# Optimization experiments

Hardware: AMD Instinct MI355X
Metric: run time of the kernel (lower is better)

## Reference

```python
import jax, jax.numpy as jnp
import numpy as np

NX, NY, D, K = 20000, 50000, 64, 8
NUM_BATCHES = 2


def _knn_np(px, py, bx, by, k):
    # Batched exact kNN via chunked squared-distance + argpartition (mirrors torch_cluster.knn under no_grad).
    pp = (px * px).sum(1)
    idx = np.empty((py.shape[0], k), np.int32)
    chunk = 4096
    for s in range(0, py.shape[0], chunk):
        q = py[s:s + chunk]
        d = (q * q).sum(1)[:, None] + pp[None, :] - 2.0 * (q @ px.T)
        d = np.where(by[s:s + chunk, None] == bx[None, :], d, np.inf)
        idx[s:s + chunk] = np.argpartition(d, k, axis=1)[:, :k].astype(np.int32)
    return idx


def setup_inputs() -> dict:
    rng = np.random.default_rng(0)
    pos_x = (rng.random((NX, 3)) * 10.0).astype(np.float32)
    pos_y = (rng.random((NY, 3)) * 10.0).astype(np.float32)
    bx = np.repeat(np.arange(NUM_BATCHES), NX // NUM_BATCHES).astype(np.int32)
    by = np.repeat(np.arange(NUM_BATCHES), NY // NUM_BATCHES).astype(np.int32)
    x_idx = _knn_np(pos_x, pos_y, bx, by, K).reshape(-1)            # [NY*K]
    y_idx = np.repeat(np.arange(NY, dtype=np.int32), K)             # [NY*K]

    key = jax.random.key(0)
    ks = jax.random.split(key, 6)

    def lin(k, fi, fo):
        return jax.random.normal(k, (fi, fo), jnp.float32) / np.sqrt(fi).astype(np.float32)

    return {
        "x": jax.random.normal(ks[0], (NX, D), jnp.float32),
        "pos_x": jnp.asarray(pos_x),
        "pos_y": jnp.asarray(pos_y),
        "x_idx": jnp.asarray(x_idx),
        "y_idx": jnp.asarray(y_idx),
        # ResnetBlockFC 1: size_in=D+3, size_h=D, size_out=D (shortcut linear, no bias)
        "W0a": lin(ks[1], D + 3, D), "b0a": jnp.zeros((D,), jnp.float32),
        "W1a": lin(ks[2], D, D),     "b1a": jnp.zeros((D,), jnp.float32),
        "Wsa": lin(ks[3], D + 3, D),
        # ResnetBlockFC 2: size_in=size_h=size_out=D (identity shortcut)
        "W0b": lin(ks[4], D, D),     "b0b": jnp.zeros((D,), jnp.float32),
        "W1b": lin(ks[5], D, D),     "b1b": jnp.zeros((D,), jnp.float32),
    }


def reference(x, pos_x, pos_y, x_idx, y_idx, W0a, b0a, W1a, b1a, Wsa, W0b, b0b, W1b, b1b):
    # gather + positional diff (diff computed under no_grad in the original)
    diff = jax.lax.stop_gradient(pos_x[x_idx] - pos_y[y_idx])        # [E, 3]
    h = jnp.concatenate([x[x_idx], diff], axis=1)                    # [E, D+3]
    # ResnetBlockFC 1: out = shortcut(h) + fc1(relu(fc0(relu(h))))
    net = jax.nn.relu(h) @ W0a + b0a
    dx = jax.nn.relu(net) @ W1a + b1a
    h = h @ Wsa + dx                                                 # [E, D]
    # ResnetBlockFC 2 (identity shortcut)
    net = jax.nn.relu(h) @ W0b + b0b
    h = h + jax.nn.relu(net) @ W1b + b1b                             # [E, D]
    # scatter-max back to query points (every query has exactly K edges)
    out = jax.ops.segment_max(h, y_idx, num_segments=NY)             # [NY, D]
    return out
```

## Files before the change

kernel.cpp:

```cpp
#include <hip/hip_runtime.h>


typedef _Float16 f16x8 __attribute__((ext_vector_type(8)));
typedef _Float16 f16x4 __attribute__((ext_vector_type(4)));
typedef float    f32x4 __attribute__((ext_vector_type(4)));

constexpr int NX     = 20000;
constexpr int NROWS  = 50000 * 8;
constexpr int NTILES = NROWS / 16;
constexpr int NFRAG  = 48;
constexpr int BW     = 8;
constexpr int BLOCK  = 64 * BW;
constexpr int TS2    = 72;

__global__ void prep_x(const float* __restrict__ x, _Float16* __restrict__ x16) {
    const int i = blockIdx.x * blockDim.x + threadIdx.x;
    if (i < NX * 16) {
        float4 v = ((const float4*)x)[i];
        f16x4 o = {(_Float16)v.x, (_Float16)v.y, (_Float16)v.z, (_Float16)v.w};
        *(f16x4*)(x16 + (size_t)i * 4) = o;
    }
}

static __device__ __forceinline__ void pack_relu(const f32x4* A, f16x8* bf) {
#pragma unroll
    for (int s = 0; s < 2; ++s) {
        f16x8 r;
#pragma unroll
        for (int e = 0; e < 8; ++e) {
            float v = A[2 * s + (e >> 2)][e & 3];
            r[e] = (_Float16)(v > 0.0f ? v : 0.0f);
        }
        bf[s] = r;
    }
}

__global__ __launch_bounds__(BLOCK, 4)
void pointnet_fused(const _Float16* __restrict__ x16,
                    const float* __restrict__ pos_x,
                    const float* __restrict__ pos_y,
                    const int*   __restrict__ x_idx,
                    const float* __restrict__ W0a, const float* __restrict__ b0a,
                    const float* __restrict__ W1a, const float* __restrict__ b1a,
                    const float* __restrict__ Wsa,
                    const float* __restrict__ W0b, const float* __restrict__ b0b,
                    const float* __restrict__ W1b, const float* __restrict__ b1b,
                    float* __restrict__ out)
{
    __shared__ __align__(16) _Float16 bfrag[NFRAG * 64 * 8];
    __shared__ __align__(16) _Float16 ebuf[BW][16 * TS2];
    __shared__ __align__(16) float    bias3f[64];
    __shared__ __align__(16) float    bias5f[64];

    const int tid = threadIdx.x;

    for (int p = tid; p < NFRAG * 64; p += BLOCK) {
        const int f = p >> 6, l = p & 63;
        const int q = l >> 4, n0 = l & 15;
        int grp, fl;
        if      (f < 12) { grp = 0; fl = f; }
        else if (f < 24) { grp = 1; fl = f - 12; }
        else if (f < 32) { grp = 2; fl = f - 24; }
        else if (f < 40) { grp = 3; fl = f - 32; }
        else             { grp = 4; fl = f - 40; }
        const int s = fl >> 2, t = fl & 3;
        const int col = t * 16 + n0;
        f16x8 v;
#pragma unroll
        for (int j = 0; j < 8; ++j) {
            const int k = 32 * s + 8 * q + j;
            float val = 0.0f;
            if      (grp == 0) val = (k < 67) ? W0a[k * 64 + col] : (k == 67 ? b0a[col] : 0.0f);
            else if (grp == 1) val = (k < 67) ? Wsa[k * 64 + col] : (k == 67 ? b1a[col] : 0.0f);
            else {
                const float* W = (grp == 2) ? W1a : (grp == 3) ? W0b : W1b;
                const int row = 32 * s + 16 * (j >> 2) + 4 * q + (j & 3);
                val = W[row * 64 + col];
            }
            v[j] = (_Float16)val;
        }
        *(f16x8*)&bfrag[p * 8] = v;
    }
    if (tid < 64)       bias3f[tid]      = b0b[tid];
    else if (tid < 128) bias5f[tid - 64] = b1b[tid - 64];
    __syncthreads();

    const int lane = tid & 63;
    const int wv   = tid >> 6;
    const int n0   = lane & 15;
    const int q    = lane >> 4;

    _Float16* eb = ebuf[wv];

    const int ey  = (lane >> 3) & 1;
    const int efg = lane & 7;
    const int esb = lane >> 4;

    const int gwave  = blockIdx.x * BW + wv;
    const int nwaves = gridDim.x * BW;

#define WFRAG(fid) (*(const f16x8*)&bfrag[(((fid) * 64) + lane) * 8])

    f16x8 hc0, hc1, hc2;
    {
        const int row = gwave * 16 + n0;
        const int xi  = x_idx[row];
        const _Float16* xp = x16 + (long)xi * 64 + q * 8;
        hc0 = *(const f16x8*)(xp);
        hc1 = *(const f16x8*)(xp + 32);
        f16x8 z = {}; hc2 = z;
        if (q == 0) {
            const int yi = row >> 3;
#pragma unroll
            for (int j = 0; j < 3; ++j)
                hc2[j] = (_Float16)(pos_x[xi * 3 + j] - pos_y[yi * 3 + j]);
            hc2[3] = (_Float16)1.0f;
        }
    }

    for (int tile = gwave; tile < NTILES; tile += nwaves) {
        const int tnx  = tile + nwaves;
        const int rown = (tnx < NTILES ? tnx : tile) * 16 + n0;
        const int xin  = x_idx[rown];
        const int yin  = rown >> 3;
        const float py0 = pos_y[yin * 3 + 0];
        const float py1 = pos_y[yin * 3 + 1];
        const float py2 = pos_y[yin * 3 + 2];

        f16x8 hr0 = hc0, hr1 = hc1, hr2 = hc2;
#pragma unroll
        for (int j = 0; j < 8; ++j) {
            hr0[j] = hr0[j] > (_Float16)0 ? hr0[j] : (_Float16)0;
            hr1[j] = hr1[j] > (_Float16)0 ? hr1[j] : (_Float16)0;
            hr2[j] = hr2[j] > (_Float16)0 ? hr2[j] : (_Float16)0;
        }

        f32x4 A1[4], A2[4];
#pragma unroll
        for (int t = 0; t < 4; ++t) {
            A1[t] = (f32x4){0.f, 0.f, 0.f, 0.f};
            A2[t] = (f32x4){0.f, 0.f, 0.f, 0.f};
        }
        {
            const f16x8 hcs[3] = {hc0, hc1, hc2};
            const f16x8 hrs[3] = {hr0, hr1, hr2};
#pragma unroll
            for (int s = 0; s < 3; ++s)
#pragma unroll
                for (int t = 0; t < 4; ++t) {
                    A2[t] = __builtin_amdgcn_mfma_f32_16x16x32_f16(WFRAG(12 + s * 4 + t), hcs[s], A2[t], 0, 0, 0);
                    A1[t] = __builtin_amdgcn_mfma_f32_16x16x32_f16(WFRAG( 0 + s * 4 + t), hrs[s], A1[t], 0, 0, 0);
                }
        }

        f16x8 hn0, hn1, hn2;
        {
            const _Float16* xp = x16 + (long)xin * 64 + q * 8;
            hn0 = *(const f16x8*)(xp);
            hn1 = *(const f16x8*)(xp + 32);
            f16x8 z = {}; hn2 = z;
            if (q == 0) {
                hn2[0] = (_Float16)(pos_x[xin * 3 + 0] - py0);
                hn2[1] = (_Float16)(pos_x[xin * 3 + 1] - py1);
                hn2[2] = (_Float16)(pos_x[xin * 3 + 2] - py2);
                hn2[3] = (_Float16)1.0f;
            }
        }

        f16x8 bf[2];
        pack_relu(A1, bf);
#pragma unroll
        for (int s = 0; s < 2; ++s)
#pragma unroll
            for (int t = 0; t < 4; ++t)
                A2[t] = __builtin_amdgcn_mfma_f32_16x16x32_f16(WFRAG(24 + s * 4 + t), bf[s], A2[t], 0, 0, 0);

        pack_relu(A2, bf);
        f32x4 A3[4];
#pragma unroll
        for (int t = 0; t < 4; ++t) A3[t] = *(const f32x4*)&bias3f[16 * t + 4 * q];
#pragma unroll
        for (int s = 0; s < 2; ++s)
#pragma unroll
            for (int t = 0; t < 4; ++t)
                A3[t] = __builtin_amdgcn_mfma_f32_16x16x32_f16(WFRAG(32 + s * 4 + t), bf[s], A3[t], 0, 0, 0);

        pack_relu(A3, bf);
#pragma unroll
        for (int s = 0; s < 2; ++s)
#pragma unroll
            for (int t = 0; t < 4; ++t)
                A2[t] = __builtin_amdgcn_mfma_f32_16x16x32_f16(WFRAG(40 + s * 4 + t), bf[s], A2[t], 0, 0, 0);

        __threadfence_block();
#pragma unroll
        for (int t = 0; t < 4; ++t) {
            f16x4 w;
#pragma unroll
            for (int r = 0; r < 4; ++r) w[r] = (_Float16)A2[t][r];
            *(f16x4*)&eb[n0 * TS2 + t * 16 + q * 4] = w;
        }
        __threadfence_block();

        const int dr0 = ey * 8 + esb * 2;
        f16x8 ra = *(const f16x8*)&eb[dr0 * TS2 + efg * 8];
        f16x8 rb = *(const f16x8*)&eb[(dr0 + 1) * TS2 + efg * 8];
#pragma unroll
        for (int e = 0; e < 8; ++e) ra[e] = ra[e] > rb[e] ? ra[e] : rb[e];
#pragma unroll
        for (int st = 0; st < 2; ++st) {
            union { f16x8 h; int i[4]; } u, v2;
            u.h = ra;
#pragma unroll
            for (int d = 0; d < 4; ++d) v2.i[d] = __shfl_xor(u.i[d], st == 0 ? 16 : 32, 64);
#pragma unroll
            for (int e = 0; e < 8; ++e) ra[e] = ra[e] > v2.h[e] ? ra[e] : v2.h[e];
        }
        if (esb == 0) {
            const f32x4 bb0 = *(const f32x4*)&bias5f[efg * 8];
            const f32x4 bb1 = *(const f32x4*)&bias5f[efg * 8 + 4];
            float4 f0 = {(float)ra[0] + bb0[0], (float)ra[1] + bb0[1],
                         (float)ra[2] + bb0[2], (float)ra[3] + bb0[3]};
            float4 f1 = {(float)ra[4] + bb1[0], (float)ra[5] + bb1[1],
                         (float)ra[6] + bb1[2], (float)ra[7] + bb1[3]};
            float* op = out + (long)(tile * 2 + ey) * 64 + efg * 8;
            *(float4*)op = f0;
            *(float4*)(op + 4) = f1;
        }

        hc0 = hn0; hc1 = hn1; hc2 = hn2;
    }
#undef WFRAG
}

extern "C" void kernel_launch(void* const* d_in, const int* in_sizes, int n_in,
                              void* d_out, int out_size, void* d_ws, size_t ws_size,
                              hipStream_t stream) {
    (void)in_sizes; (void)n_in; (void)ws_size; (void)out_size;
    _Float16* x16 = (_Float16*)d_ws;

    prep_x<<<(NX * 16 + 255) / 256, 256, 0, stream>>>((const float*)d_in[0], x16);

    pointnet_fused<<<512, BLOCK, 0, stream>>>(
        x16,
        (const float*)d_in[1],
        (const float*)d_in[2],
        (const int*)  d_in[3],
        (const float*)d_in[5],  (const float*)d_in[6],
        (const float*)d_in[7],  (const float*)d_in[8],
        (const float*)d_in[9],
        (const float*)d_in[10], (const float*)d_in[11],
        (const float*)d_in[12], (const float*)d_in[13],
        (float*)d_out);
}
```

Baseline: 124.1 us.

## Process two tiles per wave iteration, sharing weight fragment loads

Each wave now handles a pair of 16-row tiles per loop iteration. Every weight fragment read from LDS feeds two MFMAs, one per tile, and the two MFMA chains are interleaved to hide latency. This replaces the software prefetch of the next tile's gather with loading both tiles up front. It reuses the h registers for the relu'd input instead of a separate copy. The cost is higher register pressure and loss of gather/compute overlap across iterations, which could lower occupancy or expose gather latency.

After: 123.6 us. About the same (-0.4%).

```diff
diff --git a/kernel.cpp b/kernel.cpp
--- a/kernel.cpp
+++ b/kernel.cpp
@@ -8,6 +8,7 @@
 constexpr int NX     = 20000;
 constexpr int NROWS  = 50000 * 8;
 constexpr int NTILES = NROWS / 16;
+constexpr int NPAIRS = NTILES / 2;
 constexpr int NFRAG  = 48;
 constexpr int BW     = 8;
 constexpr int BLOCK  = 64 * BW;
@@ -101,134 +102,144 @@
 
 #define WFRAG(fid) (*(const f16x8*)&bfrag[(((fid) * 64) + lane) * 8])
 
-    f16x8 hc0, hc1, hc2;
-    {
-        const int row = gwave * 16 + n0;
-        const int xi  = x_idx[row];
-        const _Float16* xp = x16 + (long)xi * 64 + q * 8;
-        hc0 = *(const f16x8*)(xp);
-        hc1 = *(const f16x8*)(xp + 32);
-        f16x8 z = {}; hc2 = z;
-        if (q == 0) {
-            const int yi = row >> 3;
-#pragma unroll
-            for (int j = 0; j < 3; ++j)
-                hc2[j] = (_Float16)(pos_x[xi * 3 + j] - pos_y[yi * 3 + j]);
-            hc2[3] = (_Float16)1.0f;
-        }
-    }
-
-    for (int tile = gwave; tile < NTILES; tile += nwaves) {
-        const int tnx  = tile + nwaves;
-        const int rown = (tnx < NTILES ? tnx : tile) * 16 + n0;
-        const int xin  = x_idx[rown];
-        const int yin  = rown >> 3;
-        const float py0 = pos_y[yin * 3 + 0];
-        const float py1 = pos_y[yin * 3 + 1];
-        const float py2 = pos_y[yin * 3 + 2];
-
-        f16x8 hr0 = hc0, hr1 = hc1, hr2 = hc2;
-#pragma unroll
-        for (int j = 0; j < 8; ++j) {
-            hr0[j] = hr0[j] > (_Float16)0 ? hr0[j] : (_Float16)0;
-            hr1[j] = hr1[j] > (_Float16)0 ? hr1[j] : (_Float16)0;
-            hr2[j] = hr2[j] > (_Float16)0 ? hr2[j] : (_Float16)0;
-        }
-
-        f32x4 A1[4], A2[4];
-#pragma unroll
-        for (int t = 0; t < 4; ++t) {
-            A1[t] = (f32x4){0.f, 0.f, 0.f, 0.f};
-            A2[t] = (f32x4){0.f, 0.f, 0.f, 0.f};
-        }
-        {
-            const f16x8 hcs[3] = {hc0, hc1, hc2};
-            const f16x8 hrs[3] = {hr0, hr1, hr2};
+    for (int pr = gwave; pr < NPAIRS; pr += nwaves) {
+        const int tA = pr * 2;
+
+        f16x8 h[2][3];
+#pragma unroll
+        for (int u = 0; u < 2; ++u) {
+            const int row = (tA + u) * 16 + n0;
+            const int xi  = x_idx[row];
+            const _Float16* xp = x16 + (long)xi * 64 + q * 8;
+            h[u][0] = *(const f16x8*)(xp);
+            h[u][1] = *(const f16x8*)(xp + 32);
+            f16x8 z = {};
+            h[u][2] = z;
+            if (q == 0) {
+                const int yi = row >> 3;
+#pragma unroll
+                for (int j = 0; j < 3; ++j)
+                    h[u][2][j] = (_Float16)(pos_x[xi * 3 + j] - pos_y[yi * 3 + j]);
+                h[u][2][3] = (_Float16)1.0f;
+            }
+        }
+
+        f32x4 A2[2][4];
+#pragma unroll
+        for (int u = 0; u < 2; ++u)
+#pragma unroll
+            for (int t = 0; t < 4; ++t) A2[u][t] = (f32x4){0.f, 0.f, 0.f, 0.f};
+#pragma unroll
+        for (int s = 0; s < 3; ++s)
+#pragma unroll
+            for (int t = 0; t < 4; ++t) {
+                const f16x8 w = WFRAG(12 + s * 4 + t);
+                A2[0][t] = __builtin_amdgcn_mfma_f32_16x16x32_f16(w, h[0][s], A2[0][t], 0, 0, 0);
+                A2[1][t] = __builtin_amdgcn_mfma_f32_16x16x32_f16(w, h[1][s], A2[1][t], 0, 0, 0);
+            }
+
+#pragma unroll
+        for (int u = 0; u < 2; ++u)
 #pragma unroll
             for (int s = 0; s < 3; ++s)
 #pragma unroll
-                for (int t = 0; t < 4; ++t) {
-                    A2[t] = __builtin_amdgcn_mfma_f32_16x16x32_f16(WFRAG(12 + s * 4 + t), hcs[s], A2[t], 0, 0, 0);
-                    A1[t] = __builtin_amdgcn_mfma_f32_16x16x32_f16(WFRAG( 0 + s * 4 + t), hrs[s], A1[t], 0, 0, 0);
+                for (int j = 0; j < 8; ++j) {
+                    _Float16 v = h[u][s][j];
+                    h[u][s][j] = v > (_Float16)0 ? v : (_Float16)0;
                 }
-        }
-
-        f16x8 hn0, hn1, hn2;
-        {
-            const _Float16* xp = x16 + (long)xin * 64 + q * 8;
-            hn0 = *(const f16x8*)(xp);
-            hn1 = *(const f16x8*)(xp + 32);
-            f16x8 z = {}; hn2 = z;
-            if (q == 0) {
-                hn2[0] = (_Float16)(pos_x[xin * 3 + 0] - py0);
-                hn2[1] = (_Float16)(pos_x[xin * 3 + 1] - py1);
-                hn2[2] = (_Float16)(pos_x[xin * 3 + 2] - py2);
-                hn2[3] = (_Float16)1.0f;
-            }
-        }
-
-        f16x8 bf[2];
-        pack_relu(A1, bf);
+
+        f32x4 A1[2][4];
+#pragma unroll
+        for (int u = 0; u < 2; ++u)
+#pragma unroll
+            for (int t = 0; t < 4; ++t) A1[u][t] = (f32x4){0.f, 0.f, 0.f, 0.f};
+#pragma unroll
+        for (int s = 0; s < 3; ++s)
+#pragma unroll
+            for (int t = 0; t < 4; ++t) {
+                const f16x8 w = WFRAG(s * 4 + t);
+                A1[0][t] = __builtin_amdgcn_mfma_f32_16x16x32_f16(w, h[0][s], A1[0][t], 0, 0, 0);
+                A1[1][t] = __builtin_amdgcn_mfma_f32_16x16x32_f16(w, h[1][s], A1[1][t], 0, 0, 0);
+            }
+
+        f16x8 bf[2][2];
+#pragma unroll
+        for (int u = 0; u < 2; ++u) pack_relu(A1[u], bf[u]);
 #pragma unroll
         for (int s = 0; s < 2; ++s)
 #pragma unroll
-            for (int t = 0; t < 4; ++t)
-                A2[t] = __builtin_amdgcn_mfma_f32_16x16x32_f16(WFRAG(24 + s * 4 + t), bf[s], A2[t], 0, 0, 0);
-
-        pack_relu(A2, bf);
-        f32x4 A3[4];
-#pragma unroll
-        for (int t = 0; t < 4; ++t) A3[t] = *(const f32x4*)&bias3f[16 * t + 4 * q];
+            for (int t = 0; t < 4; ++t) {
+                const f16x8 w = WFRAG(24 + s * 4 + t);
+                A2[0][t] = __builtin_amdgcn_mfma_f32_16x16x32_f16(w, bf[0][s], A2[0][t], 0, 0, 0);
+                A2[1][t] = __builtin_amdgcn_mfma_f32_16x16x32_f16(w, bf[1][s], A2[1][t], 0, 0, 0);
+            }
+
+#pragma unroll
+        for (int u = 0; u < 2; ++u) pack_relu(A2[u], bf[u]);
+        f32x4 A3[2][4];
+#pragma unroll
+        for (int u = 0; u < 2; ++u)
+#pragma unroll
+            for (int t = 0; t < 4; ++t) A3[u][t] = *(const f32x4*)&bias3f[16 * t + 4 * q];
 #pragma unroll
         for (int s = 0; s < 2; ++s)
 #pragma unroll
-            for (int t = 0; t < 4; ++t)
-                A3[t] = __builtin_amdgcn_mfma_f32_16x16x32_f16(WFRAG(32 + s * 4 + t), bf[s], A3[t], 0, 0, 0);
-
-        pack_relu(A3, bf);
+            for (int t = 0; t < 4; ++t) {
+                const f16x8 w = WFRAG(32 + s * 4 + t);
+                A3[0][t] = __builtin_amdgcn_mfma_f32_16x16x32_f16(w, bf[0][s], A3[0][t], 0, 0, 0);
+                A3[1][t] = __builtin_amdgcn_mfma_f32_16x16x32_f16(w, bf[1][s], A3[1][t], 0, 0, 0);
+            }
+
+#pragma unroll
+        for (int u = 0; u < 2; ++u) pack_relu(A3[u], bf[u]);
 #pragma unroll
         for (int s = 0; s < 2; ++s)
 #pragma unroll
-            for (int t = 0; t < 4; ++t)
-                A2[t] = __builtin_amdgcn_mfma_f32_16x16x32_f16(WFRAG(40 + s * 4 + t), bf[s], A2[t], 0, 0, 0);
-
-        __threadfence_block();
-#pragma unroll
-        for (int t = 0; t < 4; ++t) {
-            f16x4 w;
-#pragma unroll
-            for (int r = 0; r < 4; ++r) w[r] = (_Float16)A2[t][r];
-            *(f16x4*)&eb[n0 * TS2 + t * 16 + q * 4] = w;
-        }
-        __threadfence_block();
-
-        const int dr0 = ey * 8 + esb * 2;
-        f16x8 ra = *(const f16x8*)&eb[dr0 * TS2 + efg * 8];
-        f16x8 rb = *(const f16x8*)&eb[(dr0 + 1) * TS2 + efg * 8];
-#pragma unroll
-        for (int e = 0; e < 8; ++e) ra[e] = ra[e] > rb[e] ? ra[e] : rb[e];
-#pragma unroll
-        for (int st = 0; st < 2; ++st) {
-            union { f16x8 h; int i[4]; } u, v2;
-            u.h = ra;
-#pragma unroll
-            for (int d = 0; d < 4; ++d) v2.i[d] = __shfl_xor(u.i[d], st == 0 ? 16 : 32, 64);
-#pragma unroll
-            for (int e = 0; e < 8; ++e) ra[e] = ra[e] > v2.h[e] ? ra[e] : v2.h[e];
-        }
-        if (esb == 0) {
-            const f32x4 bb0 = *(const f32x4*)&bias5f[efg * 8];
-            const f32x4 bb1 = *(const f32x4*)&bias5f[efg * 8 + 4];
-            float4 f0 = {(float)ra[0] + bb0[0], (float)ra[1] + bb0[1],
-                         (float)ra[2] + bb0[2], (float)ra[3] + bb0[3]};
-            float4 f1 = {(float)ra[4] + bb1[0], (float)ra[5] + bb1[1],
-                         (float)ra[6] + bb1[2], (float)ra[7] + bb1[3]};
-            float* op = out + (long)(tile * 2 + ey) * 64 + efg * 8;
-            *(float4*)op = f0;
-            *(float4*)(op + 4) = f1;
-        }
-
-        hc0 = hn0; hc1 = hn1; hc2 = hn2;
+            for (int t = 0; t < 4; ++t) {
+                const f16x8 w = WFRAG(40 + s * 4 + t);
+                A2[0][t] = __builtin_amdgcn_mfma_f32_16x16x32_f16(w, bf[0][s], A2[0][t], 0, 0, 0);
+                A2[1][t] = __builtin_amdgcn_mfma_f32_16x16x32_f16(w, bf[1][s], A2[1][t], 0, 0, 0);
+            }
+
+#pragma unroll
+        for (int u = 0; u < 2; ++u) {
+            const int tile = tA + u;
+            __threadfence_block();
+#pragma unroll
+            for (int t = 0; t < 4; ++t) {
+                f16x4 w;
+#pragma unroll
+                for (int r = 0; r < 4; ++r) w[r] = (_Float16)A2[u][t][r];
+                *(f16x4*)&eb[n0 * TS2 + t * 16 + q * 4] = w;
+            }
+            __threadfence_block();
+
+            const int dr0 = ey * 8 + esb * 2;
+            f16x8 ra = *(const f16x8*)&eb[dr0 * TS2 + efg * 8];
+            f16x8 rb = *(const f16x8*)&eb[(dr0 + 1) * TS2 + efg * 8];
+#pragma unroll
+            for (int e = 0; e < 8; ++e) ra[e] = ra[e] > rb[e] ? ra[e] : rb[e];
+#pragma unroll
+            for (int st = 0; st < 2; ++st) {
+                union { f16x8 h; int i[4]; } uu, v2;
+                uu.h = ra;
+#pragma unroll
+                for (int d = 0; d < 4; ++d) v2.i[d] = __shfl_xor(uu.i[d], st == 0 ? 16 : 32, 64);
+#pragma unroll
+                for (int e = 0; e < 8; ++e) ra[e] = ra[e] > v2.h[e] ? ra[e] : v2.h[e];
+            }
+            if (esb == 0) {
+                const f32x4 bb0 = *(const f32x4*)&bias5f[efg * 8];
+                const f32x4 bb1 = *(const f32x4*)&bias5f[efg * 8 + 4];
+                float4 f0 = {(float)ra[0] + bb0[0], (float)ra[1] + bb0[1],
+                             (float)ra[2] + bb0[2], (float)ra[3] + bb0[3]};
+                float4 f1 = {(float)ra[4] + bb1[0], (float)ra[5] + bb1[1],
+                             (float)ra[6] + bb1[2], (float)ra[7] + bb1[3]};
+                float* op = out + (long)(tile * 2 + ey) * 64 + efg * 8;
+                *(float4*)op = f0;
+                *(float4*)(op + 4) = f1;
+            }
+        }
     }
 #undef WFRAG
 }
```
